# Optimization experiments

Hardware: AMD Instinct MI355X
Metric: run time of the kernel (lower is better)

## Reference

```python
import jax, jax.numpy as jnp
import numpy as np

SIGMA_DATA = 16.0
ALPHA_BOND = 1.0


def safe_norm(x, axis=-1):
    # L2 norm with zero (sub)gradient at 0, matching torch.norm's behavior
    sq = jnp.sum(x * x, axis=axis)
    n = jnp.sqrt(jnp.where(sq > 0, sq, 1.0))
    return jnp.where(sq > 0, n, 0.0)


def weighted_rigid_align(x_l, xGT_l, w_l):
    # Aligns x_l onto xGT_l's frame (Kabsch with weights); output is detached.
    wm = w_l[..., None]                                   # [B,N,1]
    denom = jnp.sum(wm, axis=1, keepdims=True)
    mu = jnp.sum(wm * x_l, axis=1, keepdims=True) / denom
    muGT = jnp.sum(wm * xGT_l, axis=1, keepdims=True) / denom
    xc = x_l - mu
    xGTc = xGT_l - muGT
    # M = (w * xGT_c)^T @ x_c  -> [B,3,3]
    M = jnp.einsum('bni,bnj->bij', wm * xGTc, xc)
    U, S, Vh = jnp.linalg.svd(M)
    R = U @ Vh
    det = jnp.linalg.det(R)
    Fm = jnp.array([[1.0, 0.0, 0.0], [0.0, 1.0, 0.0], [0.0, 0.0, -1.0]], dtype=R.dtype)
    Rfix = jnp.einsum('bij,jk,bkl->bil', U, Fm, Vh)
    R = jnp.where(det[:, None, None] < 0, Rfix, R)
    xalign = xc @ jnp.swapaxes(R, -1, -2) + muGT
    return jax.lax.stop_gradient(xalign)


def diffusion_loss(xpred_l, xGT_l, ht, w_l):
    # Align ground truth onto prediction (note arg order in original forward)
    xGT_aligned = weighted_rigid_align(xGT_l, xpred_l, w_l)
    loss = jnp.sum(safe_norm(xpred_l - xGT_aligned) * w_l) / jnp.sum(w_l)
    if ALPHA_BOND > 0:
        w_pair = w_l[:, :, None] * w_l[:, None, :]                 # [B,N,N]
        d_pred = safe_norm(xpred_l[:, :, None] - xpred_l[:, None]) # [B,N,N]
        d_gt = safe_norm(xGT_l[:, :, None] - xGT_l[:, None])       # [B,N,N]
        L_bond = w_pair * (d_pred - d_gt) ** 2
        loss = loss + ALPHA_BOND * jnp.sum(L_bond) / jnp.sum(w_pair)
    return (ht ** 2 + SIGMA_DATA ** 2) / (ht + SIGMA_DATA) ** 2 * loss


def setup_inputs() -> dict:
    key = jax.random.key(0)
    k1, k2, k3, k4 = jax.random.split(key, 4)
    B, N = 4, 2048
    xpred_l = jax.random.normal(k1, (B, N, 3), dtype=jnp.float32) * 10.0
    xGT_l = jax.random.normal(k2, (B, N, 3), dtype=jnp.float32) * 10.0
    ht = jax.random.uniform(k3, (B,), dtype=jnp.float32, minval=0.1, maxval=4.0)
    w_l = jax.random.uniform(k4, (B, N), dtype=jnp.float32, minval=0.1, maxval=1.0)
    return {"xpred_l": xpred_l, "xGT_l": xGT_l, "ht": ht, "w_l": w_l}


def reference(xpred_l, xGT_l, ht, w_l):
    return diffusion_loss(xpred_l, xGT_l, ht, w_l)
```

## Files before the change

### kernel.cpp

```cpp
#include <hip/hip_runtime.h>
#include <math.h>


#define RT 256
#define CT 128
#define MAXB 8
#define MAXSTAT 1024

__global__ __launch_bounds__(RT, 4)
void k_main(const float* __restrict__ pred, const float* __restrict__ gt,
            const float* __restrict__ ht, const float* __restrict__ w,
            float* __restrict__ out, double* __restrict__ ws,
            int N, int B, unsigned total) {
    const int b    = blockIdx.z;
    const int bx   = blockIdx.x;
    const int r0   = bx * RT;
    const int c0   = blockIdx.y * CT;
    const int tid  = threadIdx.x;
    const int lane = tid & 63, wave = tid >> 6;
    const int GX   = gridDim.x;
    const unsigned linear = (blockIdx.z * gridDim.y + blockIdx.y) * GX + blockIdx.x;

    double* statsSlot = ws;
    double* bondSlot  = ws + (size_t)B * GX * 16;
    unsigned* cnt     = (unsigned*)(bondSlot + total);

    const float* p  = pred + (size_t)b * N * 3;
    const float* g  = gt   + (size_t)b * N * 3;
    const float* wb = w    + (size_t)b * N;

    __shared__ float4 sp4[CT], sg4[CT];
    __shared__ double shred[4][16];

    const int  n      = r0 + tid;
    const bool row_ok = (n < N);
    float px=0.f,py=0.f,pz=0.f,gx=0.f,gy=0.f,gz=0.f,wn=0.f;
    if (row_ok) {
        px = p[3*n]; py = p[3*n+1]; pz = p[3*n+2];
        gx = g[3*n]; gy = g[3*n+1]; gz = g[3*n+2];
        wn = wb[n];
    }

    const bool bond_active = (c0 + CT > r0 + 1) && (c0 < N);
    float bond_f = 0.0f;
    if (bond_active) {
        for (int i = tid; i < CT; i += RT) {
            int m = c0 + i;
            float4 a = make_float4(0.f,0.f,0.f,0.f), c = a;
            if (m < N) {
                a = make_float4(p[3*m], p[3*m+1], p[3*m+2], wb[m]);
                c = make_float4(g[3*m], g[3*m+1], g[3*m+2], 0.f);
            }
            sp4[i] = a; sg4[i] = c;
        }
        __syncthreads();
        if (row_ok) {
            const int cc = min(CT, N - c0);
            if (c0 >= r0 + RT) {
                for (int i = 0; i < cc; i++) {
                    float4 cp = sp4[i], cg = sg4[i];
                    float dxp=px-cp.x, dyp=py-cp.y, dzp=pz-cp.z;
                    float dxg=gx-cg.x, dyg=gy-cg.y, dzg=gz-cg.z;
                    float dp = sqrtf(dxp*dxp+dyp*dyp+dzp*dzp);
                    float dg = sqrtf(dxg*dxg+dyg*dyg+dzg*dzg);
                    float dd = dp - dg;
                    bond_f += (wn*cp.w)*(dd*dd);
                }
            } else if (n < c0 + cc - 1) {
                for (int i = 0; i < cc; i++) {
                    float4 cp = sp4[i], cg = sg4[i];
                    float dxp=px-cp.x, dyp=py-cp.y, dzp=pz-cp.z;
                    float dxg=gx-cg.x, dyg=gy-cg.y, dzg=gz-cg.z;
                    float dp = sqrtf(dxp*dxp+dyp*dyp+dzp*dzp);
                    float dg = sqrtf(dxg*dxg+dyg*dyg+dzg*dzg);
                    float dd = dp - dg;
                    float t  = (wn*cp.w)*(dd*dd);
                    bond_f += (c0 + i > n) ? t : 0.0f;
                }
            }
        }
    }
    bond_f *= 2.0f;

    if (blockIdx.y == 0) {
        double wd=wn, pxd=px,pyd=py,pzd=pz, gxd=gx,gyd=gy,gzd=gz;
        double st[16] = {wd, wd*pxd, wd*pyd, wd*pzd, wd*gxd, wd*gyd, wd*gzd,
                         wd*pxd*gxd, wd*pxd*gyd, wd*pxd*gzd,
                         wd*pyd*gxd, wd*pyd*gyd, wd*pyd*gzd,
                         wd*pzd*gxd, wd*pzd*gyd, wd*pzd*gzd};
        #pragma unroll
        for (int off = 32; off > 0; off >>= 1) {
            #pragma unroll
            for (int k = 0; k < 16; k++) st[k] += __shfl_down(st[k], off, 64);
        }
        if (lane == 0) {
            #pragma unroll
            for (int k = 0; k < 16; k++) shred[wave][k] = st[k];
        }
        __syncthreads();
        if (tid < 16) {
            double s = shred[0][tid]+shred[1][tid]+shred[2][tid]+shred[3][tid];
            unsafeAtomicAdd(&statsSlot[((size_t)b*GX + bx)*16 + tid], s);
        }
        __syncthreads();
    }

    double bd = (double)bond_f;
    #pragma unroll
    for (int off = 32; off > 0; off >>= 1) bd += __shfl_down(bd, off, 64);
    if (lane == 0) shred[wave][0] = bd;
    __syncthreads();
    if (tid == 0 && bond_active) {
        double bt = shred[0][0]+shred[1][0]+shred[2][0]+shred[3][0];
        unsafeAtomicAdd(&bondSlot[linear], bt);
    }

    __shared__ unsigned s_old;
    __syncthreads();
    if (tid == 0) s_old = atomicAdd(cnt, 1u);
    __syncthreads();
    if (s_old != total - 1u) return;

    const int nstat = B * GX * 16;
    __shared__ double sstat[MAXSTAT];
    for (int i = tid; i < nstat; i += RT)
        sstat[i] = unsafeAtomicAdd(&statsSlot[i], 0.0);

    double bsum = 0.0;
    for (unsigned i = tid; i < total; i += RT)
        bsum += unsafeAtomicAdd(&bondSlot[i], 0.0);
    #pragma unroll
    for (int off = 32; off > 0; off >>= 1) bsum += __shfl_down(bsum, off, 64);
    if (lane == 0) shred[wave][1] = bsum;
    __syncthreads();

    __shared__ double s_bond;
    __shared__ float  Rf[MAXB][15];
    __shared__ double Wd[MAXB];
    if (tid == 0) s_bond = shred[0][1]+shred[1][1]+shred[2][1]+shred[3][1];

    if (tid < B) {
        double s[16];
        for (int k = 0; k < 16; k++) {
            double acc = 0.0;
            for (int j = 0; j < GX; j++) acc += sstat[((size_t)tid*GX + j)*16 + k];
            s[k] = acc;
        }
        double W = s[0];
        double mup[3] = { s[1]/W, s[2]/W, s[3]/W };
        double mug[3] = { s[4]/W, s[5]/W, s[6]/W };
        double M[3][3];
        for (int i = 0; i < 3; i++)
            for (int j = 0; j < 3; j++)
                M[i][j] = s[7 + i*3 + j] - W * mup[i] * mug[j];

        double A[3][3];
        for (int i = 0; i < 3; i++)
            for (int j = 0; j < 3; j++) {
                double t = 0.0;
                for (int k = 0; k < 3; k++) t += M[k][i] * M[k][j];
                A[i][j] = t;
            }
        double V[3][3] = {{1,0,0},{0,1,0},{0,0,1}};
        for (int sweep = 0; sweep < 8; sweep++) {
            for (int pq = 0; pq < 3; pq++) {
                int pp_ = (pq == 2) ? 1 : 0;
                int qq_ = (pq == 0) ? 1 : 2;
                double apq = A[pp_][qq_];
                if (fabs(apq) < 1e-300) continue;
                double app = A[pp_][pp_], aqq = A[qq_][qq_];
                double theta = (aqq - app) / (2.0 * apq);
                double t = copysign(1.0, theta) / (fabs(theta) + sqrt(theta*theta + 1.0));
                double cj = 1.0 / sqrt(t*t + 1.0), sn = t * cj;
                A[pp_][pp_] = app - t * apq;
                A[qq_][qq_] = aqq + t * apq;
                A[pp_][qq_] = A[qq_][pp_] = 0.0;
                int r = 3 - pp_ - qq_;
                double arp = A[r][pp_], arq = A[r][qq_];
                A[r][pp_] = A[pp_][r] = cj*arp - sn*arq;
                A[r][qq_] = A[qq_][r] = sn*arp + cj*arq;
                for (int rr = 0; rr < 3; rr++) {
                    double vp = V[rr][pp_], vq = V[rr][qq_];
                    V[rr][pp_] = cj*vp - sn*vq;
                    V[rr][qq_] = sn*vp + cj*vq;
                }
            }
        }
        double d[3] = { A[0][0], A[1][1], A[2][2] };
        int idx[3] = {0, 1, 2};
        for (int i = 0; i < 2; i++)
            for (int j = i + 1; j < 3; j++)
                if (d[idx[j]] > d[idx[i]]) { int tt = idx[i]; idx[i] = idx[j]; idx[j] = tt; }
        double u[3][3], v[3][3];
        for (int i = 0; i < 3; i++) {
            int c_ = idx[i];
            double sv = sqrt(fmax(d[c_], 0.0));
            double inv = (sv > 1e-12) ? 1.0 / sv : 0.0;
            for (int r = 0; r < 3; r++) v[i][r] = V[r][c_];
            for (int r = 0; r < 3; r++) {
                double t = 0.0;
                for (int k = 0; k < 3; k++) t += M[r][k] * v[i][k];
                u[i][r] = t * inv;
            }
        }
        double detM = M[0][0]*(M[1][1]*M[2][2] - M[1][2]*M[2][1])
                    - M[0][1]*(M[1][0]*M[2][2] - M[1][2]*M[2][0])
                    + M[0][2]*(M[1][0]*M[2][1] - M[1][1]*M[2][0]);
        double sg2 = (detM < 0.0) ? -1.0 : 1.0;
        for (int r = 0; r < 3; r++)
            for (int cc2 = 0; cc2 < 3; cc2++)
                Rf[tid][r*3+cc2] = (float)(u[0][r]*v[0][cc2] + u[1][r]*v[1][cc2]
                                           + sg2 * u[2][r]*v[2][cc2]);
        for (int i = 0; i < 3; i++) Rf[tid][9 + i]  = (float)mup[i];
        for (int i = 0; i < 3; i++) Rf[tid][12 + i] = (float)mug[i];
        Wd[tid] = W;
    }
    __syncthreads();

    double al = 0.0;
    for (int bb = 0; bb < B; bb++) {
        float R0=Rf[bb][0], R1=Rf[bb][1], R2=Rf[bb][2];
        float R3=Rf[bb][3], R4=Rf[bb][4], R5=Rf[bb][5];
        float R6=Rf[bb][6], R7=Rf[bb][7], R8=Rf[bb][8];
        float mp0=Rf[bb][9], mp1=Rf[bb][10], mp2=Rf[bb][11];
        float mg0=Rf[bb][12], mg1=Rf[bb][13], mg2=Rf[bb][14];
        const float* pp  = pred + (size_t)bb * N * 3;
        const float* gg  = gt   + (size_t)bb * N * 3;
        const float* wwb = w    + (size_t)bb * N;
        for (int nn = tid; nn < N; nn += RT) {
            float x0 = gg[3*nn]-mg0, x1 = gg[3*nn+1]-mg1, x2 = gg[3*nn+2]-mg2;
            float ax = fmaf(R0,x0, fmaf(R1,x1, fmaf(R2,x2, mp0)));
            float ay = fmaf(R3,x0, fmaf(R4,x1, fmaf(R5,x2, mp1)));
            float az = fmaf(R6,x0, fmaf(R7,x1, fmaf(R8,x2, mp2)));
            float ex = pp[3*nn]-ax, ey = pp[3*nn+1]-ay, ez = pp[3*nn+2]-az;
            float sq = ex*ex + ey*ey + ez*ez;
            al += (double)(wwb[nn] * sqrtf(sq));
        }
    }
    #pragma unroll
    for (int off = 32; off > 0; off >>= 1) al += __shfl_down(al, off, 64);
    if (lane == 0) shred[wave][2] = al;
    __syncthreads();

    __shared__ double s_loss;
    if (tid == 0) {
        double at = shred[0][2]+shred[1][2]+shred[2][2]+shred[3][2];
        double tw = 0.0, twp = 0.0;
        for (int i = 0; i < B; i++) { double W = Wd[i]; tw += W; twp += W*W; }
        s_loss = at / tw + s_bond / twp;
    }
    __syncthreads();
    if (tid < B) {
        double h = (double)ht[tid];
        out[tid] = (float)(((h*h + 256.0) / ((h + 16.0)*(h + 16.0))) * s_loss);
    }
}

extern "C" void kernel_launch(void* const* d_in, const int* in_sizes, int n_in,
                              void* d_out, int out_size, void* d_ws, size_t ws_size,
                              hipStream_t stream) {
    const float* pred = (const float*)d_in[0];
    const float* gt   = (const float*)d_in[1];
    const float* ht   = (const float*)d_in[2];
    const float* w    = (const float*)d_in[3];
    int B = in_sizes[2];
    int N = in_sizes[3] / B;
    double* ws = (double*)d_ws;
    float* out = (float*)d_out;

    int gx = (N + RT - 1) / RT;
    int gy = (N + CT - 1) / CT;
    unsigned total = (unsigned)(gx * gy * B);
    size_t zbytes = ((size_t)B * gx * 16 + total + 2) * sizeof(double);
    hipMemsetAsync(d_ws, 0, zbytes, stream);

    k_main<<<dim3(gx, gy, B), dim3(RT), 0, stream>>>(pred, gt, ht, w, out, ws, N, B, total);
}
```

Baseline: 105.8 us.

## Split fused kernel into bond/stats kernel and tail kernel, drop memset and atomics

Replaces the last-block-done atomic counter scheme with two kernel launches: the first writes per-block partial stats and bond sums with plain stores, and a single-block second kernel reduces them, computes the Kabsch rotation and the aligned loss. This removes the hipMemsetAsync and the atomic traffic. It also halves the column tile (CT 128→64), adds unroll pragmas to the pair loops, and cuts the Jacobi sweeps from 8 to 6. The cost is an extra kernel launch, more blocks, and slightly less SVD convergence margin.

```diff
diff --git a/kernel.cpp b/kernel.cpp
--- a/kernel.cpp
+++ b/kernel.cpp
@@ -3,15 +3,14 @@
 
 
 #define RT 256
-#define CT 128
+#define CT 64
 #define MAXB 8
-#define MAXSTAT 1024
+#define MAXGX 16
 
 __global__ __launch_bounds__(RT, 4)
-void k_main(const float* __restrict__ pred, const float* __restrict__ gt,
-            const float* __restrict__ ht, const float* __restrict__ w,
-            float* __restrict__ out, double* __restrict__ ws,
-            int N, int B, unsigned total) {
+void k_bond_stats(const float* __restrict__ pred, const float* __restrict__ gt,
+                  const float* __restrict__ w, double* __restrict__ ws,
+                  int N, int B) {
     const int b    = blockIdx.z;
     const int bx   = blockIdx.x;
     const int r0   = bx * RT;
@@ -23,7 +22,6 @@
 
     double* statsSlot = ws;
     double* bondSlot  = ws + (size_t)B * GX * 16;
-    unsigned* cnt     = (unsigned*)(bondSlot + total);
 
     const float* p  = pred + (size_t)b * N * 3;
     const float* g  = gt   + (size_t)b * N * 3;
@@ -57,6 +55,7 @@
         if (row_ok) {
             const int cc = min(CT, N - c0);
             if (c0 >= r0 + RT) {
+                #pragma unroll 4
                 for (int i = 0; i < cc; i++) {
                     float4 cp = sp4[i], cg = sg4[i];
                     float dxp=px-cp.x, dyp=py-cp.y, dzp=pz-cp.z;
@@ -67,6 +66,7 @@
                     bond_f += (wn*cp.w)*(dd*dd);
                 }
             } else if (n < c0 + cc - 1) {
+                #pragma unroll 4
                 for (int i = 0; i < cc; i++) {
                     float4 cp = sp4[i], cg = sg4[i];
                     float dxp=px-cp.x, dyp=py-cp.y, dzp=pz-cp.z;
@@ -98,10 +98,9 @@
             for (int k = 0; k < 16; k++) shred[wave][k] = st[k];
         }
         __syncthreads();
-        if (tid < 16) {
-            double s = shred[0][tid]+shred[1][tid]+shred[2][tid]+shred[3][tid];
-            unsafeAtomicAdd(&statsSlot[((size_t)b*GX + bx)*16 + tid], s);
-        }
+        if (tid < 16)
+            statsSlot[((size_t)b*GX + bx)*16 + tid] =
+                shred[0][tid]+shred[1][tid]+shred[2][tid]+shred[3][tid];
         __syncthreads();
     }
 
@@ -110,42 +109,43 @@
     for (int off = 32; off > 0; off >>= 1) bd += __shfl_down(bd, off, 64);
     if (lane == 0) shred[wave][0] = bd;
     __syncthreads();
-    if (tid == 0 && bond_active) {
-        double bt = shred[0][0]+shred[1][0]+shred[2][0]+shred[3][0];
-        unsafeAtomicAdd(&bondSlot[linear], bt);
-    }
-
-    __shared__ unsigned s_old;
-    __syncthreads();
-    if (tid == 0) s_old = atomicAdd(cnt, 1u);
-    __syncthreads();
-    if (s_old != total - 1u) return;
-
-    const int nstat = B * GX * 16;
-    __shared__ double sstat[MAXSTAT];
-    for (int i = tid; i < nstat; i += RT)
-        sstat[i] = unsafeAtomicAdd(&statsSlot[i], 0.0);
+    if (tid == 0)
+        bondSlot[linear] = shred[0][0]+shred[1][0]+shred[2][0]+shred[3][0];
+}
+
+__global__ __launch_bounds__(RT, 1)
+void k_tail(const float* __restrict__ pred, const float* __restrict__ gt,
+            const float* __restrict__ ht, const float* __restrict__ w,
+            float* __restrict__ out, const double* __restrict__ ws,
+            int N, int B, int GX, unsigned total) {
+    const int tid  = threadIdx.x;
+    const int lane = tid & 63, wave = tid >> 6;
+    const double* statsSlot = ws;
+    const double* bondSlot  = ws + (size_t)B * GX * 16;
+
+    __shared__ double sstat[MAXB][16];
+    __shared__ double shred[4][16];
+    __shared__ float  Rf[MAXB][15];
+    __shared__ double Wd[MAXB];
+    __shared__ double s_bond, s_loss;
+
+    if (tid < B * 16) {
+        int bb = tid >> 4, k = tid & 15;
+        double acc = 0.0;
+        for (int j = 0; j < GX; j++) acc += statsSlot[((size_t)bb*GX + j)*16 + k];
+        sstat[bb][k] = acc;
+    }
 
     double bsum = 0.0;
-    for (unsigned i = tid; i < total; i += RT)
-        bsum += unsafeAtomicAdd(&bondSlot[i], 0.0);
+    for (unsigned i = tid; i < total; i += RT) bsum += bondSlot[i];
     #pragma unroll
     for (int off = 32; off > 0; off >>= 1) bsum += __shfl_down(bsum, off, 64);
-    if (lane == 0) shred[wave][1] = bsum;
-    __syncthreads();
-
-    __shared__ double s_bond;
-    __shared__ float  Rf[MAXB][15];
-    __shared__ double Wd[MAXB];
-    if (tid == 0) s_bond = shred[0][1]+shred[1][1]+shred[2][1]+shred[3][1];
+    if (lane == 0) shred[wave][0] = bsum;
+    __syncthreads();
+    if (tid == 0) s_bond = shred[0][0]+shred[1][0]+shred[2][0]+shred[3][0];
 
     if (tid < B) {
-        double s[16];
-        for (int k = 0; k < 16; k++) {
-            double acc = 0.0;
-            for (int j = 0; j < GX; j++) acc += sstat[((size_t)tid*GX + j)*16 + k];
-            s[k] = acc;
-        }
+        const double* s = sstat[tid];
         double W = s[0];
         double mup[3] = { s[1]/W, s[2]/W, s[3]/W };
         double mug[3] = { s[4]/W, s[5]/W, s[6]/W };
@@ -153,7 +153,6 @@
         for (int i = 0; i < 3; i++)
             for (int j = 0; j < 3; j++)
                 M[i][j] = s[7 + i*3 + j] - W * mup[i] * mug[j];
-
         double A[3][3];
         for (int i = 0; i < 3; i++)
             for (int j = 0; j < 3; j++) {
@@ -162,7 +161,7 @@
                 A[i][j] = t;
             }
         double V[3][3] = {{1,0,0},{0,1,0},{0,0,1}};
-        for (int sweep = 0; sweep < 8; sweep++) {
+        for (int sweep = 0; sweep < 6; sweep++) {
             for (int pq = 0; pq < 3; pq++) {
                 int pp_ = (pq == 2) ? 1 : 0;
                 int qq_ = (pq == 0) ? 1 : 2;
@@ -222,7 +221,7 @@
         float R0=Rf[bb][0], R1=Rf[bb][1], R2=Rf[bb][2];
         float R3=Rf[bb][3], R4=Rf[bb][4], R5=Rf[bb][5];
         float R6=Rf[bb][6], R7=Rf[bb][7], R8=Rf[bb][8];
-        float mp0=Rf[bb][9], mp1=Rf[bb][10], mp2=Rf[bb][11];
+        float mp0=Rf[bb][9],  mp1=Rf[bb][10], mp2=Rf[bb][11];
         float mg0=Rf[bb][12], mg1=Rf[bb][13], mg2=Rf[bb][14];
         const float* pp  = pred + (size_t)bb * N * 3;
         const float* gg  = gt   + (size_t)bb * N * 3;
@@ -239,12 +238,10 @@
     }
     #pragma unroll
     for (int off = 32; off > 0; off >>= 1) al += __shfl_down(al, off, 64);
-    if (lane == 0) shred[wave][2] = al;
-    __syncthreads();
-
-    __shared__ double s_loss;
+    if (lane == 0) shred[wave][1] = al;
+    __syncthreads();
     if (tid == 0) {
-        double at = shred[0][2]+shred[1][2]+shred[2][2]+shred[3][2];
+        double at = shred[0][1]+shred[1][1]+shred[2][1]+shred[3][1];
         double tw = 0.0, twp = 0.0;
         for (int i = 0; i < B; i++) { double W = Wd[i]; tw += W; twp += W*W; }
         s_loss = at / tw + s_bond / twp;
@@ -271,8 +268,7 @@
     int gx = (N + RT - 1) / RT;
     int gy = (N + CT - 1) / CT;
     unsigned total = (unsigned)(gx * gy * B);
-    size_t zbytes = ((size_t)B * gx * 16 + total + 2) * sizeof(double);
-    hipMemsetAsync(d_ws, 0, zbytes, stream);
-
-    k_main<<<dim3(gx, gy, B), dim3(RT), 0, stream>>>(pred, gt, ht, w, out, ws, N, B, total);
+
+    k_bond_stats<<<dim3(gx, gy, B), dim3(RT), 0, stream>>>(pred, gt, w, ws, N, B);
+    k_tail<<<dim3(1), dim3(RT), 0, stream>>>(pred, gt, ht, w, out, ws, N, B, gx, total);
 }
```

After: 100.5 us. 4.9% less time.
